# Optimization experiments

Hardware: AMD Instinct MI355X
Metric: run time of the kernel (lower is better)

Reference implementation:

```python
import jax, jax.numpy as jnp
import numpy as np

IN_F = 4096
OUT_F = 4096
SPLIT_F = 410   # ceil(4096 * 0.1)
NUM_PARTS = 10  # ceil(4096 / 410)


def setup_inputs() -> dict:
    key = jax.random.key(0)
    ks = jax.random.split(key, 7)
    s = 1.0 / np.sqrt(IN_F)
    sn = 1.0 / np.sqrt(NUM_PARTS)
    return {
        'x': jax.random.normal(ks[0], (2, 2048, IN_F), dtype=jnp.float32),
        'Wsel': jax.random.uniform(ks[1], (NUM_PARTS, IN_F), jnp.float32, -s, s),
        'bsel': jax.random.uniform(ks[2], (NUM_PARTS,), jnp.float32, -s, s),
        'Wexp': jax.random.uniform(ks[3], (IN_F, NUM_PARTS), jnp.float32, -sn, sn),
        'bexp': jax.random.uniform(ks[4], (IN_F,), jnp.float32, -sn, sn),
        'Wfc': jax.random.uniform(ks[5], (SPLIT_F, IN_F), jnp.float32, -s, s),
        'bfc': jax.random.uniform(ks[6], (SPLIT_F,), jnp.float32, -s, s),
        'out_features': OUT_F,
    }


def reference(x, Wsel, bsel, Wexp, bexp, Wfc, bfc, out_features):
    # selector: sx[..., n]
    sx = jnp.einsum('bsi,ni->bsn', x, Wsel) + bsel
    # expander(diag_embed(sx)): px[..., n, f] = sx[..., n] * Wexp[f, n] + bexp[f]
    # (diag matrix never materialized; mathematically identical)
    px = sx[..., :, None] * Wexp.T[None, None, :, :] + bexp  # [b, s, n, in]
    xx = x[..., None, :] + px                                # broadcast-add of x
    y = jnp.einsum('bsni,fi->bsnf', xx, Wfc) + bfc           # splitfc, [b, s, n, sf]
    y = y.reshape(y.shape[0], y.shape[1], -1)                # (n sf) flatten
    return y[..., :out_features]
```

## Files before the change

kernel.cpp:

```cpp
#include <hip/hip_runtime.h>
#include <hip/hip_bf16.h>
#include <stdint.h>

#define TKS    4096
#define KD     4096
#define NSF    410
#define NPARTS 10
#define OUTF   4096

typedef unsigned short u16;
typedef __attribute__((ext_vector_type(8))) short bf16x8;
typedef __attribute__((ext_vector_type(4))) float f32x4;

#define WS_XB  0
#define WS_BSW ((size_t)TKS * KD * 2)
#define WS_SX  (WS_BSW + (size_t)448 * 512 * 8 * 2)
#define WS_GC  (WS_SX + (size_t)TKS * NPARTS * 4)

__device__ inline u16 f2bf(float f) {
    union { __hip_bfloat16 b; u16 u; } cv;
    cv.b = __float2bfloat16(f);
    return cv.u;
}

__device__ inline int g_row(int g) { int s = g >> 6; return (s >> 2) * 32 + (s & 1) * 16 + (g & 15); }
__device__ inline int g_col(int g) { int s = g >> 6; return ((s >> 1) & 1) * 32 + ((g >> 4) & 3) * 8; }

__global__ __launch_bounds__(256) void prep(const float* __restrict__ x,
                                            const float* __restrict__ Wsel,
                                            const float* __restrict__ bsel,
                                            const float* __restrict__ Wexp,
                                            const float* __restrict__ bexp,
                                            const float* __restrict__ Wfc,
                                            const float* __restrict__ bfc,
                                            u16* __restrict__ xb,
                                            u16* __restrict__ bsw,
                                            float* __restrict__ sxb,
                                            float* __restrict__ gc) {
    const int bid = blockIdx.x;
    const int tid = threadIdx.x;

    if (bid < 128) {
        const int b3 = bid;
        const int w = tid >> 6, lane = tid & 63;
        const int t0 = b3 * 32 + w * 8;
        float acc[8][NPARTS];
#pragma unroll
        for (int t = 0; t < 8; ++t)
#pragma unroll
            for (int n = 0; n < NPARTS; ++n) acc[t][n] = 0.f;

        for (int k4 = 0; k4 < 16; ++k4) {
            const int k = k4 * 256 + lane * 4;
            float4 ws[NPARTS];
#pragma unroll
            for (int n = 0; n < NPARTS; ++n)
                ws[n] = *(const float4*)&Wsel[(size_t)n * KD + k];
#pragma unroll
            for (int t = 0; t < 8; ++t) {
                float4 xv = *(const float4*)&x[(size_t)(t0 + t) * KD + k];
#pragma unroll
                for (int n = 0; n < NPARTS; ++n)
                    acc[t][n] += xv.x * ws[n].x + xv.y * ws[n].y
                               + xv.z * ws[n].z + xv.w * ws[n].w;
            }
        }
#pragma unroll
        for (int s = 1; s < 64; s <<= 1)
#pragma unroll
            for (int t = 0; t < 8; ++t)
#pragma unroll
                for (int n = 0; n < NPARTS; ++n)
                    acc[t][n] += __shfl_xor(acc[t][n], s);
        if (lane == 0) {
#pragma unroll
            for (int t = 0; t < 8; ++t)
#pragma unroll
                for (int n = 0; n < NPARTS; ++n)
                    sxb[(size_t)(t0 + t) * NPARTS + n] = acc[t][n] + bsel[n];
        }

    } else if (bid < 142) {
        const int b4 = bid - 128;
        const int w = tid >> 6, lane = tid & 63;
        const int f0 = b4 * 32 + w * 8;
        float acc[8][11];
#pragma unroll
        for (int t = 0; t < 8; ++t)
#pragma unroll
            for (int n = 0; n < 11; ++n) acc[t][n] = 0.f;

        for (int k4 = 0; k4 < 16; ++k4) {
            const int k = k4 * 256 + lane * 4;
            float we[4][11];
#pragma unroll
            for (int j = 0; j < 4; ++j) {
#pragma unroll
                for (int n = 0; n < NPARTS; ++n)
                    we[j][n] = Wexp[(size_t)(k + j) * NPARTS + n];
                we[j][10] = bexp[k + j];
            }
#pragma unroll
            for (int t = 0; t < 8; ++t) {
                const int f = f0 + t;
                float4 xv = (f < NSF) ? *(const float4*)&Wfc[(size_t)f * KD + k]
                                      : make_float4(0.f, 0.f, 0.f, 0.f);
#pragma unroll
                for (int n = 0; n < 11; ++n)
                    acc[t][n] += xv.x * we[0][n] + xv.y * we[1][n]
                               + xv.z * we[2][n] + xv.w * we[3][n];
            }
        }
#pragma unroll
        for (int s = 1; s < 64; s <<= 1)
#pragma unroll
            for (int t = 0; t < 8; ++t)
#pragma unroll
                for (int n = 0; n < 11; ++n)
                    acc[t][n] += __shfl_xor(acc[t][n], s);
        if (lane == 0) {
#pragma unroll
            for (int t = 0; t < 8; ++t) {
                const int f = f0 + t;
#pragma unroll
                for (int n = 0; n < NPARTS; ++n)
                    gc[(size_t)f * 12 + n] = (f < NSF) ? acc[t][n] : 0.f;
                gc[(size_t)f * 12 + 10] = (f < NSF) ? acc[t][10] + bfc[f] : 0.f;
            }
        }

    } else if (bid < 8334) {
        const int b1 = bid - 142;
        const int kt = b1 & 63, tb = b1 >> 6;
        const int g = tid;
        const int slot = g >> 6;
        const int row = (slot & 1) * 16 + (g & 15);
        const int col = (slot >> 1) * 32 + ((g >> 4) & 3) * 8;
        const float* src = x + (size_t)(tb * 32 + row) * KD + kt * 64 + col;
        float4 v0 = *(const float4*)src;
        float4 v1 = *(const float4*)(src + 4);
        u16 h[8] = { f2bf(v0.x), f2bf(v0.y), f2bf(v0.z), f2bf(v0.w),
                     f2bf(v1.x), f2bf(v1.y), f2bf(v1.z), f2bf(v1.w) };
        *(uint4*)&xb[((size_t)(tb * 64 + kt) * 256 + g) * 8] = *(uint4*)h;

    } else {
        const int b2 = bid - 8334;
        const int kt = b2 & 63, rb = b2 >> 6;
        u16* tout = bsw + ((size_t)(rb * 64 + kt) * 512) * 8;
#pragma unroll
        for (int j = 0; j < 2; ++j) {
            const int g = j * 256 + tid;
            const int r = rb * 64 + g_row(g);
            uint4 pk = make_uint4(0u, 0u, 0u, 0u);
            if (r < NSF) {
                const float* src = Wfc + (size_t)r * KD + kt * 64 + g_col(g);
                float4 v0 = *(const float4*)src;
                float4 v1 = *(const float4*)(src + 4);
                u16 h[8] = { f2bf(v0.x), f2bf(v0.y), f2bf(v0.z), f2bf(v0.w),
                             f2bf(v1.x), f2bf(v1.y), f2bf(v1.z), f2bf(v1.w) };
                pk = *(uint4*)h;
            }
            *(uint4*)&tout[(size_t)g * 8] = pk;
        }
    }
}

#define A_IDX(kt, mi, ks) ((((size_t)(tb * 2 + ((mi) >> 1)) * 64 + (size_t)(kt)) * 256 \
                            + ((ks) * 2 + ((mi) & 1)) * 64 + lane) * 8)
#define B_IDX(kt, nj, ks) (((size_t)(fb * 64 + (kt)) * 512 \
                            + (wf * 4 + (ks) * 2 + (nj)) * 64 + lane) * 8)

__global__ __launch_bounds__(256, 2) void main_kernel(const u16* __restrict__ xb,
                                                      const u16* __restrict__ bsw,
                                                      const float* __restrict__ sxb,
                                                      const float* __restrict__ gc,
                                                      float* __restrict__ out) {
    __shared__ float red[4][4][16][34];
    __shared__ float sxt[64][NPARTS];
    __shared__ float gt[32][12];

    const int tid = threadIdx.x;
    const int f2 = blockIdx.x >> 6;
    const int tb = blockIdx.x & 63;
    const int lane = tid & 63;
    const int kh = tid >> 6;
    const int q = lane >> 4, ml = lane & 15;
    const int fb = f2 >> 1, wf = f2 & 1;

    f32x4 acc[4][2];
#pragma unroll
    for (int mi = 0; mi < 4; ++mi)
#pragma unroll
        for (int nj = 0; nj < 2; ++nj) acc[mi][nj] = (f32x4){0.f,0.f,0.f,0.f};

    bf16x8 fa[4][4], fbv[4][2];

#define LOADAB(p, kt, ks) do {                                            \
        _Pragma("unroll")                                                 \
        for (int mi = 0; mi < 4; ++mi)                                    \
            fa[p][mi] = *(const bf16x8*)&xb[A_IDX((kt), mi, (ks))];       \
        _Pragma("unroll")                                                 \
        for (int nj = 0; nj < 2; ++nj)                                    \
            fbv[p][nj] = *(const bf16x8*)&bsw[B_IDX((kt), nj, (ks))];     \
    } while (0)

#define MFMAS(p) do {                                                     \
        _Pragma("unroll")                                                 \
        for (int mi = 0; mi < 4; ++mi)                                    \
            _Pragma("unroll")                                             \
            for (int nj = 0; nj < 2; ++nj)                                \
                acc[mi][nj] = __builtin_amdgcn_mfma_f32_16x16x32_bf16(    \
                    fa[p][mi], fbv[p][nj], acc[mi][nj], 0, 0, 0);         \
    } while (0)

#define LD(p, s) LOADAB((p), kh * 16 + ((s) >> 1), (s) & 1)

    LD(0, 0); LD(1, 1); LD(2, 2);
    __builtin_amdgcn_sched_group_barrier(0x020, 18, 0);
#pragma unroll
    for (int s = 0; s < 32; ++s) {
        if (s + 3 < 32) LD((s + 3) & 3, s + 3);
        MFMAS(s & 3);
        if (s + 3 < 32)
            __builtin_amdgcn_sched_group_barrier(0x020, 6, 0);
        __builtin_amdgcn_sched_group_barrier(0x008, 8, 0);
    }
#undef LD
#undef LOADAB
#undef MFMAS

#pragma unroll
    for (int mi = 0; mi < 4; ++mi)
#pragma unroll
        for (int nj = 0; nj < 2; ++nj)
#pragma unroll
            for (int r = 0; r < 4; ++r)
                red[mi][kh][q * 4 + r][nj * 16 + ml] = acc[mi][nj][r];

    for (int i = tid; i < 64 * NPARTS; i += 256)
        sxt[i / NPARTS][i % NPARTS] = sxb[((size_t)tb * 64 + i / NPARTS) * NPARTS + i % NPARTS];
    for (int i = tid; i < 32 * 11; i += 256)
        gt[i / 11][i % 11] = gc[((size_t)f2 * 32 + i / 11) * 12 + i % 11];
    __syncthreads();

#pragma unroll
    for (int nj = 0; nj < 2; ++nj) {
        const int fl = nj * 16 + ml;
        const int fg = f2 * 32 + fl;
        if (fg >= NSF) continue;
        const float cv = gt[fl][10];
        float gv[NPARTS];
#pragma unroll
        for (int n = 0; n < NPARTS; ++n) gv[n] = gt[fl][n];
#pragma unroll
        for (int r = 0; r < 4; ++r) {
            const int tl = kh * 16 + q * 4 + r;
            const float v = red[kh][0][q * 4 + r][fl] + red[kh][1][q * 4 + r][fl]
                          + red[kh][2][q * 4 + r][fl] + red[kh][3][q * 4 + r][fl];
            const float av = v + cv;
            float* orow = out + (size_t)(tb * 64 + tl) * OUTF;
#pragma unroll
            for (int n = 0; n < NPARTS; ++n) {
                const int j = n * NSF + fg;
                if (j < OUTF) orow[j] = av + sxt[tl][n] * gv[n];
            }
        }
    }
}

extern "C" void kernel_launch(void* const* d_in, const int* in_sizes, int n_in,
                              void* d_out, int out_size, void* d_ws, size_t ws_size,
                              hipStream_t stream) {
    const float* x    = (const float*)d_in[0];
    const float* Wsel = (const float*)d_in[1];
    const float* bsel = (const float*)d_in[2];
    const float* Wexp = (const float*)d_in[3];
    const float* bexp = (const float*)d_in[4];
    const float* Wfc  = (const float*)d_in[5];
    const float* bfc  = (const float*)d_in[6];
    float* out = (float*)d_out;

    char* ws = (char*)d_ws;
    u16* xb    = (u16*)(ws + WS_XB);
    u16* bsw   = (u16*)(ws + WS_BSW);
    float* sxb = (float*)(ws + WS_SX);
    float* gcv = (float*)(ws + WS_GC);

    prep<<<dim3(128 + 14 + 8192 + 448), dim3(256), 0, stream>>>(
        x, Wsel, bsel, Wexp, bexp, Wfc, bfc, xb, bsw, sxb, gcv);
    main_kernel<<<dim3(13 * 64), dim3(256), 0, stream>>>(xb, bsw, sxb, gcv, out);
}
```

Baseline: 215.9 us.

## Split expansion epilogue into separate coalesced float4 expand kernel

The GEMM kernel now writes only the 410-column base result into the first columns of each output row. A new expand kernel reads that back per 4-token block and writes all 4096 output columns with coalesced float4 stores, adding the selector and bias terms. This replaces the scattered 10-way strided scalar stores in the GEMM epilogue. The cost is an extra kernel launch plus a round trip of the base tile through global memory.

```diff
diff --git a/kernel.cpp b/kernel.cpp
--- a/kernel.cpp
+++ b/kernel.cpp
@@ -172,12 +172,8 @@
 
 __global__ __launch_bounds__(256, 2) void main_kernel(const u16* __restrict__ xb,
                                                       const u16* __restrict__ bsw,
-                                                      const float* __restrict__ sxb,
-                                                      const float* __restrict__ gc,
                                                       float* __restrict__ out) {
     __shared__ float red[4][4][16][34];
-    __shared__ float sxt[64][NPARTS];
-    __shared__ float gt[32][12];
 
     const int tid = threadIdx.x;
     const int f2 = blockIdx.x >> 6;
@@ -236,11 +232,6 @@
 #pragma unroll
             for (int r = 0; r < 4; ++r)
                 red[mi][kh][q * 4 + r][nj * 16 + ml] = acc[mi][nj][r];
-
-    for (int i = tid; i < 64 * NPARTS; i += 256)
-        sxt[i / NPARTS][i % NPARTS] = sxb[((size_t)tb * 64 + i / NPARTS) * NPARTS + i % NPARTS];
-    for (int i = tid; i < 32 * 11; i += 256)
-        gt[i / 11][i % 11] = gc[((size_t)f2 * 32 + i / 11) * 12 + i % 11];
     __syncthreads();
 
 #pragma unroll
@@ -248,22 +239,56 @@
         const int fl = nj * 16 + ml;
         const int fg = f2 * 32 + fl;
         if (fg >= NSF) continue;
-        const float cv = gt[fl][10];
-        float gv[NPARTS];
-#pragma unroll
-        for (int n = 0; n < NPARTS; ++n) gv[n] = gt[fl][n];
 #pragma unroll
         for (int r = 0; r < 4; ++r) {
             const int tl = kh * 16 + q * 4 + r;
             const float v = red[kh][0][q * 4 + r][fl] + red[kh][1][q * 4 + r][fl]
                           + red[kh][2][q * 4 + r][fl] + red[kh][3][q * 4 + r][fl];
-            const float av = v + cv;
-            float* orow = out + (size_t)(tb * 64 + tl) * OUTF;
-#pragma unroll
-            for (int n = 0; n < NPARTS; ++n) {
-                const int j = n * NSF + fg;
-                if (j < OUTF) orow[j] = av + sxt[tl][n] * gv[n];
-            }
+            out[(size_t)(tb * 64 + tl) * OUTF + fg] = v;
+        }
+    }
+}
+
+__global__ __launch_bounds__(256) void expand(const float* __restrict__ sxb,
+                                              const float* __restrict__ gc,
+                                              float* out) {
+    __shared__ float Ct[4][412];
+    __shared__ float sxl[4][NPARTS];
+    const int tid = threadIdx.x;
+    const int t0 = blockIdx.x * 4;
+
+    int   ns[4][4], fgs[4][4];
+    float gv[4][4], cv[4][4];
+#pragma unroll
+    for (int g = 0; g < 4; ++g)
+#pragma unroll
+        for (int e = 0; e < 4; ++e) {
+            const int j = g * 1024 + tid * 4 + e;
+            const int n = j / NSF;
+            const int fg = j - n * NSF;
+            ns[g][e] = n; fgs[g][e] = fg;
+            gv[g][e] = gc[(size_t)fg * 12 + n];
+            cv[g][e] = gc[(size_t)fg * 12 + 10];
+        }
+
+    for (int i = tid; i < 4 * NSF; i += 256)
+        Ct[i / NSF][i % NSF] = out[(size_t)(t0 + i / NSF) * OUTF + (i % NSF)];
+    if (tid < 4 * NPARTS)
+        sxl[tid / NPARTS][tid % NPARTS] =
+            sxb[(size_t)(t0 + tid / NPARTS) * NPARTS + tid % NPARTS];
+    __syncthreads();
+
+#pragma unroll
+    for (int r = 0; r < 4; ++r) {
+        float* orow = out + (size_t)(t0 + r) * OUTF;
+#pragma unroll
+        for (int g = 0; g < 4; ++g) {
+            float4 v;
+            v.x = Ct[r][fgs[g][0]] + sxl[r][ns[g][0]] * gv[g][0] + cv[g][0];
+            v.y = Ct[r][fgs[g][1]] + sxl[r][ns[g][1]] * gv[g][1] + cv[g][1];
+            v.z = Ct[r][fgs[g][2]] + sxl[r][ns[g][2]] * gv[g][2] + cv[g][2];
+            v.w = Ct[r][fgs[g][3]] + sxl[r][ns[g][3]] * gv[g][3] + cv[g][3];
+            *(float4*)&orow[g * 1024 + tid * 4] = v;
         }
     }
 }
@@ -288,5 +313,6 @@
 
     prep<<<dim3(128 + 14 + 8192 + 448), dim3(256), 0, stream>>>(
         x, Wsel, bsel, Wexp, bexp, Wfc, bfc, xb, bsw, sxb, gcv);
-    main_kernel<<<dim3(13 * 64), dim3(256), 0, stream>>>(xb, bsw, sxb, gcv, out);
-}
+    main_kernel<<<dim3(13 * 64), dim3(256), 0, stream>>>(xb, bsw, out);
+    expand<<<dim3(1024), dim3(256), 0, stream>>>(sxb, gcv, out);
+}
```

Measured after the change: 206.5 us. 4.3% less time.
